# Kernel optimization log

Measured on AMD Instinct MI355X. Metric: run time of the kernel, lower is better.

Reference implementation:

```python
import jax, jax.numpy as jnp
import numpy as np

# CLEVR-scale dims
B, N, DF, DE, DV, H, NC, QV, L = 128, 36, 512, 256, 512, 256, 28, 2000, 5


def _lin(key, fan_in, fan_out):
    k1, _ = jax.random.split(key)
    w = jax.random.normal(k1, (fan_in, fan_out), jnp.float32) * np.sqrt(2.0 / fan_in)  # kaiming
    b = jnp.zeros((fan_out,), jnp.float32)
    return w, b


def setup_inputs() -> dict:
    key = jax.random.key(0)
    ks = jax.random.split(key, 12)
    node_feats = jax.random.normal(ks[0], (B, N, DF), jnp.float32)
    edge_feats = jax.random.normal(ks[1], (B, N, N, DE), jnp.float32)
    programs = jax.random.randint(ks[2], (B, L), 0, 10)
    program_inputs = jax.random.randint(ks[3], (B, L), 0, QV)
    W_n1, b_n1 = _lin(ks[4], DF, H)
    W_n2, b_n2 = _lin(ks[5], H, DV)
    W_e1, b_e1 = _lin(ks[6], DE, H)
    W_e2, b_e2 = _lin(ks[7], H, DV)
    W_q, b_q = _lin(ks[8], DV, DV)
    W_c1, b_c1 = _lin(ks[9], DV, H)
    W_c2, b_c2 = _lin(ks[10], H, NC)
    word_emb = jax.random.normal(ks[11], (QV, DV), jnp.float32) / np.sqrt(DV)
    return dict(node_feats=node_feats, edge_feats=edge_feats,
                W_n1=W_n1, b_n1=b_n1, W_n2=W_n2, b_n2=b_n2,
                W_e1=W_e1, b_e1=b_e1, W_e2=W_e2, b_e2=b_e2,
                W_q=W_q, b_q=b_q, W_c1=W_c1, b_c1=b_c1,
                W_c2=W_c2, b_c2=b_c2, word_emb=word_emb,
                programs=programs, program_inputs=program_inputs)


def _mlp(x, W1, b1, W2, b2):
    return jax.nn.relu(x @ W1 + b1) @ W2 + b2


def reference(node_feats, edge_feats, W_n1, b_n1, W_n2, b_n2,
              W_e1, b_e1, W_e2, b_e2, W_q, b_q,
              W_c1, b_c1, W_c2, b_c2, word_emb,
              programs, program_inputs):
    # Fixed representative program (executed in reverse order like the torch code):
    # scene -> filter -> relate -> filter -> query -> classifier
    del programs
    scale = 1.0 / np.sqrt(DV)
    nf = _mlp(node_feats, W_n1, b_n1, W_n2, b_n2)      # [B,N,DV]  map_node_feat_to_v
    ef = _mlp(edge_feats, W_e1, b_e1, W_e2, b_e2)      # [B,N,N,DV] map_edge_feat_to_v
    q = word_emb[program_inputs]                        # [B,L,DV]  word_embedding lookup
    # scene: attention of ones over nodes
    attn = jnp.ones(nf.shape[:2], nf.dtype)             # [B,N]
    # filter (AttentionModule): gate node attention by query-node similarity
    attn = attn * jax.nn.sigmoid(jnp.einsum('bnd,bd->bn', nf, q[:, 3]) * scale)
    # relate (RelateModule): transfer attention along query-weighted edges
    weit = jax.nn.sigmoid(jnp.einsum('bijd,bd->bij', ef, q[:, 2]) * scale)  # [B,N,N]
    attn = jnp.clip(jnp.einsum('bi,bij->bj', attn, weit), 0.0, 1.0)
    # filter again
    attn = attn * jax.nn.sigmoid(jnp.einsum('bnd,bd->bn', nf, q[:, 1]) * scale)
    # query (QueryModule): attention-pooled node feature gated by query, projected
    attn_n = attn / (attn.sum(-1, keepdims=True) + 1e-8)
    pooled = jnp.einsum('bn,bnd->bd', attn_n, nf)        # [B,DV]
    out = jax.nn.relu((pooled * q[:, 0]) @ W_q + b_q)    # [B,DV]
    # classifier
    return jax.nn.relu(out @ W_c1 + b_c1) @ W_c2 + b_c2  # [B,NC]
```

## Files before the change

### kernel.cpp

```cpp
#include <hip/hip_runtime.h>
#include <math.h>

#define BB 128
#define NN 36
#define DF 512
#define DE 256
#define DV 512
#define HH 256
#define NCC 28
#define LQ 5
#define NE 1296
#define SCALE 0.04419417382415922f

typedef __bf16 bf16_8 __attribute__((ext_vector_type(8)));
typedef __bf16 bf16_4 __attribute__((ext_vector_type(4)));
typedef float  f32_4  __attribute__((ext_vector_type(4)));

__device__ __forceinline__ float sigmoidf_(float x){ return 1.0f/(1.0f + expf(-x)); }
__device__ __forceinline__ float reluf_(float x){ return x > 0.f ? x : 0.f; }

__global__ __launch_bounds__(256) void k_pack_all(
    const float* __restrict__ W_n1, const float* __restrict__ W_n2,
    const float* __restrict__ W_q,  const float* __restrict__ W_c1,
    const float* __restrict__ W_e1,
    __bf16* __restrict__ Pn1h, __bf16* __restrict__ Pn1l,
    __bf16* __restrict__ Pn2h, __bf16* __restrict__ Pn2l,
    __bf16* __restrict__ Pqh,  __bf16* __restrict__ Pql,
    __bf16* __restrict__ Pc1h, __bf16* __restrict__ Pc1l,
    __bf16* __restrict__ Peh)
{
    int bid = blockIdx.x;
    const float* W; __bf16 *Ph, *Pl; int N, base;
    if (bid < 64)       { W=W_n1; Ph=Pn1h; Pl=Pn1l; N=256; base=0;   }
    else if (bid < 128) { W=W_n2; Ph=Pn2h; Pl=Pn2l; N=512; base=64;  }
    else if (bid < 256) { W=W_q;  Ph=Pqh;  Pl=Pql;  N=512; base=128; }
    else if (bid < 320) { W=W_c1; Ph=Pc1h; Pl=Pc1l; N=256; base=256; }
    else                { W=W_e1; Ph=Peh;  Pl=nullptr; N=256; base=320; }
    int g = (bid-base)*256 + threadIdx.x;
    int lane = g & 63, slot = g >> 6;
    int NT = N >> 4;
    int nt = slot % NT, kt = slot / NT;
    int krow = kt*32 + (lane>>4)*8, ncol = nt*16 + (lane&15);
    #pragma unroll
    for (int j=0;j<8;j++){
        float w = W[(size_t)(krow+j)*N + ncol];
        __bf16 hi = (__bf16)w;
        Ph[(size_t)g*8+j] = hi;
        if (Pl) Pl[(size_t)g*8+j] = (__bf16)(w - (float)hi);
    }
}

__global__ __launch_bounds__(256) void k_prep(
    const float* __restrict__ word_emb, const int* __restrict__ program_inputs,
    const float* __restrict__ W_e2, const float* __restrict__ b_e2,
    float* __restrict__ qws, float* __restrict__ ve, float* __restrict__ se)
{
    int b = blockIdx.x, t = threadIdx.x, wv = t>>6, lane = t&63;
    int idx[4];
    #pragma unroll
    for (int k=0;k<4;k++) idx[k] = program_inputs[b*LQ + k];
    #pragma unroll
    for (int k=0;k<4;k++){
        qws[((size_t)(b*4+k))*DV + t]       = word_emb[(size_t)idx[k]*DV + t];
        qws[((size_t)(b*4+k))*DV + t + 256] = word_emb[(size_t)idx[k]*DV + t + 256];
    }
    const float* q2p = word_emb + (size_t)idx[2]*DV + lane*8;
    float4 qa = *(const float4*)q2p, qb = *(const float4*)(q2p+4);
    for (int i=0;i<64;i++){
        int h = wv*64 + i;
        const float* wr = W_e2 + (size_t)h*DV + lane*8;
        float4 a = *(const float4*)wr, c = *(const float4*)(wr+4);
        float p = a.x*qa.x + a.y*qa.y + a.z*qa.z + a.w*qa.w
                + c.x*qb.x + c.y*qb.y + c.z*qb.z + c.w*qb.w;
        #pragma unroll
        for (int off=32; off; off>>=1) p += __shfl_xor(p, off, 64);
        if (lane==0) ve[b*HH + h] = p;
    }
    float pp = b_e2[t]*word_emb[(size_t)idx[2]*DV + t]
             + b_e2[t+256]*word_emb[(size_t)idx[2]*DV + t + 256];
    __shared__ float red[4];
    #pragma unroll
    for (int off=32; off; off>>=1) pp += __shfl_down(pp, off, 64);
    if ((t&63)==0) red[t>>6] = pp;
    __syncthreads();
    if (t==0) se[b] = red[0]+red[1]+red[2]+red[3];
}

__global__ __launch_bounds__(256) void k_node(
    const float* __restrict__ X,
    const __bf16* __restrict__ W1h, const __bf16* __restrict__ W1l,
    const float* __restrict__ b1,
    const __bf16* __restrict__ W2h, const __bf16* __restrict__ W2l,
    const float* __restrict__ b2,
    float* __restrict__ nf)
{
    __shared__ __align__(16) __bf16 xh[16*512];
    __shared__ __align__(16) __bf16 xl[16*512];
    __shared__ __align__(16) __bf16 hh[8*64*8];
    __shared__ __align__(16) __bf16 hl[8*64*8];
    int r0 = blockIdx.x*16, t = threadIdx.x, wv = t>>6, lane = t&63;

    #pragma unroll
    for (int i=0;i<8;i++){
        int linear = t + i*256;
        int row = linear >> 7, c4 = (linear & 127)*4;
        float4 f = *(const float4*)(X + (size_t)(r0+row)*DF + c4);
        int kt = c4 >> 5, lane2 = ((c4 & 31) >> 3)*16 + row, j2 = c4 & 7;
        bf16_4 h, l;
        h[0]=(__bf16)f.x; l[0]=(__bf16)(f.x-(float)h[0]);
        h[1]=(__bf16)f.y; l[1]=(__bf16)(f.y-(float)h[1]);
        h[2]=(__bf16)f.z; l[2]=(__bf16)(f.z-(float)h[2]);
        h[3]=(__bf16)f.w; l[3]=(__bf16)(f.w-(float)h[3]);
        int off = (kt*64 + lane2)*8 + j2;
        *(bf16_4*)&xh[off] = h;
        *(bf16_4*)&xl[off] = l;
    }
    __syncthreads();

    f32_4 zero = {0.f,0.f,0.f,0.f};
    f32_4 acc1[4];
    #pragma unroll
    for (int nt=0;nt<4;nt++) acc1[nt] = zero;
    for (int kt=0; kt<16; kt++){
        bf16_8 ah = *(const bf16_8*)&xh[(kt*64+lane)*8];
        bf16_8 al = *(const bf16_8*)&xl[(kt*64+lane)*8];
        #pragma unroll
        for (int nt=0;nt<4;nt++){
            size_t bo = ((size_t)(kt*16 + wv*4+nt)*64 + lane)*8;
            bf16_8 bh = *(const bf16_8*)(W1h + bo);
            bf16_8 bl = *(const bf16_8*)(W1l + bo);
            acc1[nt] = __builtin_amdgcn_mfma_f32_16x16x32_bf16(ah, bh, acc1[nt], 0,0,0);
            acc1[nt] = __builtin_amdgcn_mfma_f32_16x16x32_bf16(al, bh, acc1[nt], 0,0,0);
            acc1[nt] = __builtin_amdgcn_mfma_f32_16x16x32_bf16(ah, bl, acc1[nt], 0,0,0);
        }
    }
    int q = lane>>4, c = lane&15;
    #pragma unroll
    for (int nt=0;nt<4;nt++){
        int col = wv*64 + nt*16 + c;
        float bias = b1[col];
        int kt2 = col>>5, j2 = col&7;
        int lbase = ((col&31)>>3)*16;
        #pragma unroll
        for (int r=0;r<4;r++){
            int row = q*4 + r;
            float v = reluf_(acc1[nt][r] + bias);
            __bf16 hi = (__bf16)v;
            int off = (kt2*64 + lbase + row)*8 + j2;
            hh[off] = hi;
            hl[off] = (__bf16)(v - (float)hi);
        }
    }
    __syncthreads();

    f32_4 acc2[8];
    #pragma unroll
    for (int nt=0;nt<8;nt++) acc2[nt] = zero;
    for (int kt=0; kt<8; kt++){
        bf16_8 ah = *(const bf16_8*)&hh[(kt*64+lane)*8];
        bf16_8 al = *(const bf16_8*)&hl[(kt*64+lane)*8];
        #pragma unroll
        for (int nt=0;nt<8;nt++){
            size_t bo = ((size_t)(kt*32 + wv*8+nt)*64 + lane)*8;
            bf16_8 bh = *(const bf16_8*)(W2h + bo);
            bf16_8 bl = *(const bf16_8*)(W2l + bo);
            acc2[nt] = __builtin_amdgcn_mfma_f32_16x16x32_bf16(ah, bh, acc2[nt], 0,0,0);
            acc2[nt] = __builtin_amdgcn_mfma_f32_16x16x32_bf16(al, bh, acc2[nt], 0,0,0);
            acc2[nt] = __builtin_amdgcn_mfma_f32_16x16x32_bf16(ah, bl, acc2[nt], 0,0,0);
        }
    }
    #pragma unroll
    for (int nt=0;nt<8;nt++){
        int col = wv*128 + nt*16 + c;
        float bias = b2[col];
        #pragma unroll
        for (int r=0;r<4;r++){
            int row = q*4 + r;
            nf[(size_t)(r0+row)*DV + col] = acc2[nt][r] + bias;
        }
    }
}

__global__ __launch_bounds__(256) void k_edge(
    const float* __restrict__ E, const __bf16* __restrict__ Wp,
    const float* __restrict__ b_e1, const float* __restrict__ ve,
    const float* __restrict__ se, float* __restrict__ weit)
{
    constexpr int LDW = DE + 8;
    __shared__ __align__(16) __bf16 as[48*LDW];
    __shared__ float red[4][48];
    int bx = blockIdx.x;
    int b = bx / 27, tile = bx % 27;
    int e0 = tile*48;
    int t = threadIdx.x, wv = t>>6, lane = t&63;
    const float* Eb = E + ((size_t)b*NE + e0)*DE;

    #pragma unroll
    for (int i=0;i<6;i++){
        int cch = t + i*256;
        int row = cch >> 5, cc = cch & 31;
        const float* src = Eb + (size_t)row*DE + cc*8;
        float4 f0 = *(const float4*)(src);
        float4 f1 = *(const float4*)(src+4);
        bf16_8 v;
        v[0]=(__bf16)f0.x; v[1]=(__bf16)f0.y; v[2]=(__bf16)f0.z; v[3]=(__bf16)f0.w;
        v[4]=(__bf16)f1.x; v[5]=(__bf16)f1.y; v[6]=(__bf16)f1.z; v[7]=(__bf16)f1.w;
        *(bf16_8*)&as[row*LDW + cc*8] = v;
    }
    __syncthreads();

    f32_4 zero = {0.f,0.f,0.f,0.f};
    f32_4 acc[3][4];
    #pragma unroll
    for (int mt=0;mt<3;mt++)
        #pragma unroll
        for (int nt=0;nt<4;nt++) acc[mt][nt] = zero;

    int arow = lane & 15, ako = (lane>>4)*8;
    for (int kt=0; kt<8; kt++){
        bf16_8 afrag[3];
        #pragma unroll
        for (int mt=0;mt<3;mt++)
            afrag[mt] = *(const bf16_8*)&as[(mt*16 + arow)*LDW + kt*32 + ako];
        #pragma unroll
        for (int nt=0;nt<4;nt++){
            bf16_8 bfrag = *(const bf16_8*)(Wp + ((size_t)(kt*16 + (wv*4+nt))*64 + lane)*8);
            #pragma unroll
            for (int mt=0;mt<3;mt++)
                acc[mt][nt] = __builtin_amdgcn_mfma_f32_16x16x32_bf16(afrag[mt], bfrag, acc[mt][nt], 0,0,0);
        }
    }

    float ves[4], be[4];
    #pragma unroll
    for (int nt=0;nt<4;nt++){
        int n = wv*64 + nt*16 + (lane&15);
        ves[nt] = ve[b*HH + n];
        be[nt]  = b_e1[n];
    }
    float part[3][4];
    #pragma unroll
    for (int mt=0;mt<3;mt++)
        #pragma unroll
        for (int r=0;r<4;r++){
            float s = 0.f;
            #pragma unroll
            for (int nt=0;nt<4;nt++)
                s = fmaf(reluf_(acc[mt][nt][r] + be[nt]), ves[nt], s);
            part[mt][r] = s;
        }
    #pragma unroll
    for (int off=1; off<16; off<<=1)
        #pragma unroll
        for (int mt=0;mt<3;mt++)
            #pragma unroll
            for (int r=0;r<4;r++)
                part[mt][r] += __shfl_xor(part[mt][r], off, 64);
    if ((lane&15)==0){
        int g = lane>>4;
        #pragma unroll
        for (int mt=0;mt<3;mt++)
            #pragma unroll
            for (int r=0;r<4;r++)
                red[wv][mt*16 + g*4 + r] = part[mt][r];
    }
    __syncthreads();
    if (t < 48){
        float logit = red[0][t]+red[1][t]+red[2][t]+red[3][t] + se[b];
        weit[(size_t)b*NE + e0 + t] = sigmoidf_(logit * SCALE);
    }
}

__global__ __launch_bounds__(256) void k_attn(
    const float* __restrict__ nf, const float* __restrict__ qws,
    const float* __restrict__ weit, float* __restrict__ xws)
{
    int b = blockIdx.x, t = threadIdx.x;
    int wv = t>>6, lane = t&63;
    __shared__ float a1[NN], a2[NN], a3[NN];
    __shared__ float denom;
    const float* nfb = nf + (size_t)b*NN*DV;
    const float* q0 = qws + ((size_t)(b*4+0))*DV;
    const float* q1 = qws + ((size_t)(b*4+1))*DV;
    const float* q3 = qws + ((size_t)(b*4+3))*DV;

    for (int i=wv; i<NN; i+=4){
        const float* row = nfb + (size_t)i*DV + lane*8;
        const float* qq  = q3 + lane*8;
        float4 x0 = *(const float4*)row, x1 = *(const float4*)(row+4);
        float4 y0 = *(const float4*)qq,  y1 = *(const float4*)(qq+4);
        float p = x0.x*y0.x + x0.y*y0.y + x0.z*y0.z + x0.w*y0.w
                + x1.x*y1.x + x1.y*y1.y + x1.z*y1.z + x1.w*y1.w;
        #pragma unroll
        for (int off=32; off; off>>=1) p += __shfl_xor(p, off, 64);
        if (lane==0) a1[i] = sigmoidf_(p*SCALE);
    }
    __syncthreads();
    if (t < NN){
        const float* wrow = weit + (size_t)b*NE;
        float s = 0.f;
        for (int i=0;i<NN;i++) s = fmaf(a1[i], wrow[i*NN + t], s);
        a2[t] = fminf(fmaxf(s, 0.f), 1.f);
    }
    __syncthreads();
    for (int i=wv; i<NN; i+=4){
        const float* row = nfb + (size_t)i*DV + lane*8;
        const float* qq  = q1 + lane*8;
        float4 x0 = *(const float4*)row, x1 = *(const float4*)(row+4);
        float4 y0 = *(const float4*)qq,  y1 = *(const float4*)(qq+4);
        float p = x0.x*y0.x + x0.y*y0.y + x0.z*y0.z + x0.w*y0.w
                + x1.x*y1.x + x1.y*y1.y + x1.z*y1.z + x1.w*y1.w;
        #pragma unroll
        for (int off=32; off; off>>=1) p += __shfl_xor(p, off, 64);
        if (lane==0) a3[i] = a2[i]*sigmoidf_(p*SCALE);
    }
    __syncthreads();
    if (t==0){
        float s = 0.f;
        for (int i=0;i<NN;i++) s += a3[i];
        denom = 1.f/(s + 1e-8f);
    }
    __syncthreads();
    float p0=0.f, p1=0.f;
    for (int i=0;i<NN;i++){
        float a = a3[i]*denom;
        p0 = fmaf(a, nfb[(size_t)i*DV + t], p0);
        p1 = fmaf(a, nfb[(size_t)i*DV + t + 256], p1);
    }
    xws[(size_t)b*DV + t]       = p0*q0[t];
    xws[(size_t)b*DV + t + 256] = p1*q0[t+256];
}

__global__ __launch_bounds__(256) void k_head(
    const float* __restrict__ xws,
    const __bf16* __restrict__ Wqh, const __bf16* __restrict__ Wql,
    const float* __restrict__ b_q,
    const __bf16* __restrict__ Wc1h, const __bf16* __restrict__ Wc1l,
    const float* __restrict__ b_c1,
    const float* __restrict__ W_c2, const float* __restrict__ b_c2,
    float* __restrict__ out)
{
    __shared__ __align__(16) char smem[65536];
    __bf16* xh = (__bf16*)smem;
    __bf16* xl = xh + 8192;
    __bf16* oh = (__bf16*)(smem + 32768);
    __bf16* ol = oh + 8192;
    float* hbuf  = (float*)smem;
    float* wc2s  = (float*)(smem + 32768);

    int r0 = blockIdx.x*16, t = threadIdx.x, wv = t>>6, lane = t&63;
    int q = lane>>4, c = lane&15;

    #pragma unroll
    for (int i=0;i<8;i++){
        int linear = t + i*256;
        int row = linear >> 7, c4 = (linear & 127)*4;
        float4 f = *(const float4*)(xws + (size_t)(r0+row)*DV + c4);
        int kt = c4 >> 5, lane2 = ((c4 & 31) >> 3)*16 + row, j2 = c4 & 7;
        bf16_4 h, l;
        h[0]=(__bf16)f.x; l[0]=(__bf16)(f.x-(float)h[0]);
        h[1]=(__bf16)f.y; l[1]=(__bf16)(f.y-(float)h[1]);
        h[2]=(__bf16)f.z; l[2]=(__bf16)(f.z-(float)h[2]);
        h[3]=(__bf16)f.w; l[3]=(__bf16)(f.w-(float)h[3]);
        int off = (kt*64 + lane2)*8 + j2;
        *(bf16_4*)&xh[off] = h;
        *(bf16_4*)&xl[off] = l;
    }
    __syncthreads();

    f32_4 zero = {0.f,0.f,0.f,0.f};
    f32_4 acc[8];
    #pragma unroll
    for (int nt=0;nt<8;nt++) acc[nt] = zero;
    for (int kt=0; kt<16; kt++){
        bf16_8 ah = *(const bf16_8*)&xh[(kt*64+lane)*8];
        bf16_8 al = *(const bf16_8*)&xl[(kt*64+lane)*8];
        #pragma unroll
        for (int nt=0;nt<8;nt++){
            size_t bo = ((size_t)(kt*32 + wv*8+nt)*64 + lane)*8;
            bf16_8 bh = *(const bf16_8*)(Wqh + bo);
            bf16_8 bl = *(const bf16_8*)(Wql + bo);
            acc[nt] = __builtin_amdgcn_mfma_f32_16x16x32_bf16(ah, bh, acc[nt], 0,0,0);
            acc[nt] = __builtin_amdgcn_mfma_f32_16x16x32_bf16(al, bh, acc[nt], 0,0,0);
            acc[nt] = __builtin_amdgcn_mfma_f32_16x16x32_bf16(ah, bl, acc[nt], 0,0,0);
        }
    }
    #pragma unroll
    for (int nt=0;nt<8;nt++){
        int col = wv*128 + nt*16 + c;
        float bias = b_q[col];
        int kt2 = col>>5, j2 = col&7;
        int lbase = ((col&31)>>3)*16;
        #pragma unroll
        for (int r=0;r<4;r++){
            int row = q*4 + r;
            float v = reluf_(acc[nt][r] + bias);
            __bf16 hi = (__bf16)v;
            int off = (kt2*64 + lbase + row)*8 + j2;
            oh[off] = hi;
            ol[off] = (__bf16)(v - (float)hi);
        }
    }
    __syncthreads();

    f32_4 acc2[4];
    #pragma unroll
    for (int nt=0;nt<4;nt++) acc2[nt] = zero;
    for (int kt=0; kt<16; kt++){
        bf16_8 ah = *(const bf16_8*)&oh[(kt*64+lane)*8];
        bf16_8 al = *(const bf16_8*)&ol[(kt*64+lane)*8];
        #pragma unroll
        for (int nt=0;nt<4;nt++){
            size_t bo = ((size_t)(kt*16 + wv*4+nt)*64 + lane)*8;
            bf16_8 bh = *(const bf16_8*)(Wc1h + bo);
            bf16_8 bl = *(const bf16_8*)(Wc1l + bo);
            acc2[nt] = __builtin_amdgcn_mfma_f32_16x16x32_bf16(ah, bh, acc2[nt], 0,0,0);
            acc2[nt] = __builtin_amdgcn_mfma_f32_16x16x32_bf16(al, bh, acc2[nt], 0,0,0);
            acc2[nt] = __builtin_amdgcn_mfma_f32_16x16x32_bf16(ah, bl, acc2[nt], 0,0,0);
        }
    }
    __syncthreads();
    #pragma unroll
    for (int nt=0;nt<4;nt++){
        int col = wv*64 + nt*16 + c;
        float bias = b_c1[col];
        #pragma unroll
        for (int r=0;r<4;r++){
            int row = q*4 + r;
            hbuf[row*264 + col] = reluf_(acc2[nt][r] + bias);
        }
    }
    for (int i=t; i<1792; i+=256)
        ((float4*)wc2s)[i] = ((const float4*)W_c2)[i];
    __syncthreads();

    for (int idx=t; idx<16*NCC; idx+=256){
        int row = idx / NCC, cc = idx - row*NCC;
        float s = b_c2[cc];
        for (int k=0;k<HH;k++)
            s = fmaf(hbuf[row*264 + k], wc2s[k*NCC + cc], s);
        out[(size_t)(r0+row)*NCC + cc] = s;
    }
}

extern "C" void kernel_launch(void* const* d_in, const int* in_sizes, int n_in,
                              void* d_out, int out_size, void* d_ws, size_t ws_size,
                              hipStream_t stream)
{
    const float* node_feats = (const float*)d_in[0];
    const float* edge_feats = (const float*)d_in[1];
    const float* W_n1 = (const float*)d_in[2];
    const float* b_n1 = (const float*)d_in[3];
    const float* W_n2 = (const float*)d_in[4];
    const float* b_n2 = (const float*)d_in[5];
    const float* W_e1 = (const float*)d_in[6];
    const float* b_e1 = (const float*)d_in[7];
    const float* W_e2 = (const float*)d_in[8];
    const float* b_e2 = (const float*)d_in[9];
    const float* W_q  = (const float*)d_in[10];
    const float* b_q  = (const float*)d_in[11];
    const float* W_c1 = (const float*)d_in[12];
    const float* b_c1 = (const float*)d_in[13];
    const float* W_c2 = (const float*)d_in[14];
    const float* b_c2 = (const float*)d_in[15];
    const float* word_emb = (const float*)d_in[16];
    const int* program_inputs = (const int*)d_in[18];

    char* ws = (char*)d_ws;
    float* qws  = (float*)ws; ws += (size_t)BB*4*DV*4;
    float* ve   = (float*)ws; ws += (size_t)BB*HH*4;
    float* se   = (float*)ws; ws += 512;
    float* xws  = (float*)ws; ws += (size_t)BB*DV*4;
    __bf16* Pn1h = (__bf16*)ws; ws += (size_t)DF*HH*2;
    __bf16* Pn1l = (__bf16*)ws; ws += (size_t)DF*HH*2;
    __bf16* Pn2h = (__bf16*)ws; ws += (size_t)HH*DV*2;
    __bf16* Pn2l = (__bf16*)ws; ws += (size_t)HH*DV*2;
    __bf16* Pqh  = (__bf16*)ws; ws += (size_t)DV*DV*2;
    __bf16* Pql  = (__bf16*)ws; ws += (size_t)DV*DV*2;
    __bf16* Pc1h = (__bf16*)ws; ws += (size_t)DV*HH*2;
    __bf16* Pc1l = (__bf16*)ws; ws += (size_t)DV*HH*2;
    __bf16* Peh  = (__bf16*)ws; ws += (size_t)DE*HH*2;
    float* nf   = (float*)ws; ws += (size_t)BB*NN*DV*4;
    float* weit = (float*)ws; ws += (size_t)BB*NE*4;

    k_pack_all<<<352, 256, 0, stream>>>(W_n1, W_n2, W_q, W_c1, W_e1,
                                        Pn1h, Pn1l, Pn2h, Pn2l, Pqh, Pql, Pc1h, Pc1l, Peh);
    k_prep<<<BB, 256, 0, stream>>>(word_emb, program_inputs, W_e2, b_e2, qws, ve, se);
    k_node<<<(BB*NN)/16, 256, 0, stream>>>(node_feats, Pn1h, Pn1l, b_n1, Pn2h, Pn2l, b_n2, nf);
    k_edge<<<BB*27, 256, 0, stream>>>(edge_feats, Peh, b_e1, ve, se, weit);
    k_attn<<<BB, 256, 0, stream>>>(nf, qws, weit, xws);
    k_head<<<BB/16, 256, 0, stream>>>(xws, Pqh, Pql, b_q, Pc1h, Pc1l, b_c1, W_c2, b_c2,
                                      (float*)d_out);
}
```

Measured before the change: 457.5 us.

## Load MFMA A-fragments directly from global memory and move classifier output to MFMA

The node, edge and head kernels now load fp32 input rows straight from global memory into registers in MFMA fragment layout and convert them there, instead of staging through LDS with a barrier. The edge kernel uses nontemporal loads for the large streamed edge tensor. The final classifier layer, previously a scalar fp32 loop over LDS, now uses split-bf16 MFMA with W_c2 packed (padded to 32 columns) in the pack kernel. The aim is lower LDS traffic, fewer syncs and better occupancy, at the cost of less coalesced global access patterns.

After: 529.8 us. +15.8%, slower.

```diff
diff --git a/kernel.cpp b/kernel.cpp
--- a/kernel.cpp
+++ b/kernel.cpp
@@ -19,23 +19,41 @@
 __device__ __forceinline__ float sigmoidf_(float x){ return 1.0f/(1.0f + expf(-x)); }
 __device__ __forceinline__ float reluf_(float x){ return x > 0.f ? x : 0.f; }
 
+__device__ __forceinline__ bf16_8 cvt8(f32_4 f0, f32_4 f1){
+    bf16_8 v;
+    #pragma unroll
+    for (int i=0;i<4;i++){ v[i] = (__bf16)f0[i]; v[i+4] = (__bf16)f1[i]; }
+    return v;
+}
+__device__ __forceinline__ void split8(f32_4 f0, f32_4 f1, bf16_8& h, bf16_8& l){
+    #pragma unroll
+    for (int i=0;i<4;i++){
+        __bf16 hi = (__bf16)f0[i];
+        h[i] = hi; l[i] = (__bf16)(f0[i] - (float)hi);
+        __bf16 hi2 = (__bf16)f1[i];
+        h[i+4] = hi2; l[i+4] = (__bf16)(f1[i] - (float)hi2);
+    }
+}
+
 __global__ __launch_bounds__(256) void k_pack_all(
     const float* __restrict__ W_n1, const float* __restrict__ W_n2,
     const float* __restrict__ W_q,  const float* __restrict__ W_c1,
-    const float* __restrict__ W_e1,
+    const float* __restrict__ W_e1, const float* __restrict__ W_c2,
     __bf16* __restrict__ Pn1h, __bf16* __restrict__ Pn1l,
     __bf16* __restrict__ Pn2h, __bf16* __restrict__ Pn2l,
     __bf16* __restrict__ Pqh,  __bf16* __restrict__ Pql,
     __bf16* __restrict__ Pc1h, __bf16* __restrict__ Pc1l,
-    __bf16* __restrict__ Peh)
+    __bf16* __restrict__ Peh,
+    __bf16* __restrict__ Pc2h, __bf16* __restrict__ Pc2l)
 {
     int bid = blockIdx.x;
-    const float* W; __bf16 *Ph, *Pl; int N, base;
-    if (bid < 64)       { W=W_n1; Ph=Pn1h; Pl=Pn1l; N=256; base=0;   }
-    else if (bid < 128) { W=W_n2; Ph=Pn2h; Pl=Pn2l; N=512; base=64;  }
-    else if (bid < 256) { W=W_q;  Ph=Pqh;  Pl=Pql;  N=512; base=128; }
-    else if (bid < 320) { W=W_c1; Ph=Pc1h; Pl=Pc1l; N=256; base=256; }
-    else                { W=W_e1; Ph=Peh;  Pl=nullptr; N=256; base=320; }
+    const float* W; __bf16 *Ph, *Pl; int N, base, realN;
+    if (bid < 64)       { W=W_n1; Ph=Pn1h; Pl=Pn1l; N=256; base=0;   realN=256; }
+    else if (bid < 128) { W=W_n2; Ph=Pn2h; Pl=Pn2l; N=512; base=64;  realN=512; }
+    else if (bid < 256) { W=W_q;  Ph=Pqh;  Pl=Pql;  N=512; base=128; realN=512; }
+    else if (bid < 320) { W=W_c1; Ph=Pc1h; Pl=Pc1l; N=256; base=256; realN=256; }
+    else if (bid < 352) { W=W_e1; Ph=Peh;  Pl=nullptr; N=256; base=320; realN=256; }
+    else                { W=W_c2; Ph=Pc2h; Pl=Pc2l; N=32;  base=352; realN=28;  }
     int g = (bid-base)*256 + threadIdx.x;
     int lane = g & 63, slot = g >> 6;
     int NT = N >> 4;
@@ -43,7 +61,7 @@
     int krow = kt*32 + (lane>>4)*8, ncol = nt*16 + (lane&15);
     #pragma unroll
     for (int j=0;j<8;j++){
-        float w = W[(size_t)(krow+j)*N + ncol];
+        float w = (ncol < realN) ? W[(size_t)(krow+j)*realN + ncol] : 0.f;
         __bf16 hi = (__bf16)w;
         Ph[(size_t)g*8+j] = hi;
         if (Pl) Pl[(size_t)g*8+j] = (__bf16)(w - (float)hi);
@@ -65,13 +83,13 @@
         qws[((size_t)(b*4+k))*DV + t + 256] = word_emb[(size_t)idx[k]*DV + t + 256];
     }
     const float* q2p = word_emb + (size_t)idx[2]*DV + lane*8;
-    float4 qa = *(const float4*)q2p, qb = *(const float4*)(q2p+4);
+    f32_4 qa = *(const f32_4*)q2p, qb = *(const f32_4*)(q2p+4);
     for (int i=0;i<64;i++){
         int h = wv*64 + i;
         const float* wr = W_e2 + (size_t)h*DV + lane*8;
-        float4 a = *(const float4*)wr, c = *(const float4*)(wr+4);
-        float p = a.x*qa.x + a.y*qa.y + a.z*qa.z + a.w*qa.w
-                + c.x*qb.x + c.y*qb.y + c.z*qb.z + c.w*qb.w;
+        f32_4 a = *(const f32_4*)wr, c = *(const f32_4*)(wr+4);
+        float p = a[0]*qa[0] + a[1]*qa[1] + a[2]*qa[2] + a[3]*qa[3]
+                + c[0]*qb[0] + c[1]*qb[1] + c[2]*qb[2] + c[3]*qb[3];
         #pragma unroll
         for (int off=32; off; off>>=1) p += __shfl_xor(p, off, 64);
         if (lane==0) ve[b*HH + h] = p;
@@ -94,36 +112,22 @@
     const float* __restrict__ b2,
     float* __restrict__ nf)
 {
-    __shared__ __align__(16) __bf16 xh[16*512];
-    __shared__ __align__(16) __bf16 xl[16*512];
-    __shared__ __align__(16) __bf16 hh[8*64*8];
-    __shared__ __align__(16) __bf16 hl[8*64*8];
+    __shared__ __align__(16) __bf16 hh[4096];
+    __shared__ __align__(16) __bf16 hl[4096];
     int r0 = blockIdx.x*16, t = threadIdx.x, wv = t>>6, lane = t&63;
-
-    #pragma unroll
-    for (int i=0;i<8;i++){
-        int linear = t + i*256;
-        int row = linear >> 7, c4 = (linear & 127)*4;
-        float4 f = *(const float4*)(X + (size_t)(r0+row)*DF + c4);
-        int kt = c4 >> 5, lane2 = ((c4 & 31) >> 3)*16 + row, j2 = c4 & 7;
-        bf16_4 h, l;
-        h[0]=(__bf16)f.x; l[0]=(__bf16)(f.x-(float)h[0]);
-        h[1]=(__bf16)f.y; l[1]=(__bf16)(f.y-(float)h[1]);
-        h[2]=(__bf16)f.z; l[2]=(__bf16)(f.z-(float)h[2]);
-        h[3]=(__bf16)f.w; l[3]=(__bf16)(f.w-(float)h[3]);
-        int off = (kt*64 + lane2)*8 + j2;
-        *(bf16_4*)&xh[off] = h;
-        *(bf16_4*)&xl[off] = l;
-    }
-    __syncthreads();
-
+    int m = lane&15, kc = lane>>4;
+    int q = lane>>4, c = lane&15;
+
+    const float* xr = X + (size_t)(r0+m)*DF + kc*8;
     f32_4 zero = {0.f,0.f,0.f,0.f};
     f32_4 acc1[4];
     #pragma unroll
     for (int nt=0;nt<4;nt++) acc1[nt] = zero;
     for (int kt=0; kt<16; kt++){
-        bf16_8 ah = *(const bf16_8*)&xh[(kt*64+lane)*8];
-        bf16_8 al = *(const bf16_8*)&xl[(kt*64+lane)*8];
+        f32_4 f0 = *(const f32_4*)(xr + kt*32);
+        f32_4 f1 = *(const f32_4*)(xr + kt*32 + 4);
+        bf16_8 ah, al;
+        split8(f0, f1, ah, al);
         #pragma unroll
         for (int nt=0;nt<4;nt++){
             size_t bo = ((size_t)(kt*16 + wv*4+nt)*64 + lane)*8;
@@ -134,7 +138,6 @@
             acc1[nt] = __builtin_amdgcn_mfma_f32_16x16x32_bf16(ah, bl, acc1[nt], 0,0,0);
         }
     }
-    int q = lane>>4, c = lane&15;
     #pragma unroll
     for (int nt=0;nt<4;nt++){
         int col = wv*64 + nt*16 + c;
@@ -186,28 +189,16 @@
     const float* __restrict__ b_e1, const float* __restrict__ ve,
     const float* __restrict__ se, float* __restrict__ weit)
 {
-    constexpr int LDW = DE + 8;
-    __shared__ __align__(16) __bf16 as[48*LDW];
     __shared__ float red[4][48];
     int bx = blockIdx.x;
     int b = bx / 27, tile = bx % 27;
     int e0 = tile*48;
     int t = threadIdx.x, wv = t>>6, lane = t&63;
-    const float* Eb = E + ((size_t)b*NE + e0)*DE;
-
-    #pragma unroll
-    for (int i=0;i<6;i++){
-        int cch = t + i*256;
-        int row = cch >> 5, cc = cch & 31;
-        const float* src = Eb + (size_t)row*DE + cc*8;
-        float4 f0 = *(const float4*)(src);
-        float4 f1 = *(const float4*)(src+4);
-        bf16_8 v;
-        v[0]=(__bf16)f0.x; v[1]=(__bf16)f0.y; v[2]=(__bf16)f0.z; v[3]=(__bf16)f0.w;
-        v[4]=(__bf16)f1.x; v[5]=(__bf16)f1.y; v[6]=(__bf16)f1.z; v[7]=(__bf16)f1.w;
-        *(bf16_8*)&as[row*LDW + cc*8] = v;
-    }
-    __syncthreads();
+    int m = lane&15, kc = lane>>4;
+    const float* base = E + ((size_t)b*NE + e0)*DE + kc*8;
+    const float* rp0 = base + (size_t)(0*16 + m)*DE;
+    const float* rp1 = base + (size_t)(1*16 + m)*DE;
+    const float* rp2 = base + (size_t)(2*16 + m)*DE;
 
     f32_4 zero = {0.f,0.f,0.f,0.f};
     f32_4 acc[3][4];
@@ -216,25 +207,27 @@
         #pragma unroll
         for (int nt=0;nt<4;nt++) acc[mt][nt] = zero;
 
-    int arow = lane & 15, ako = (lane>>4)*8;
     for (int kt=0; kt<8; kt++){
-        bf16_8 afrag[3];
-        #pragma unroll
-        for (int mt=0;mt<3;mt++)
-            afrag[mt] = *(const bf16_8*)&as[(mt*16 + arow)*LDW + kt*32 + ako];
+        bf16_8 af[3];
+        af[0] = cvt8(__builtin_nontemporal_load((const f32_4*)(rp0 + kt*32)),
+                     __builtin_nontemporal_load((const f32_4*)(rp0 + kt*32 + 4)));
+        af[1] = cvt8(__builtin_nontemporal_load((const f32_4*)(rp1 + kt*32)),
+                     __builtin_nontemporal_load((const f32_4*)(rp1 + kt*32 + 4)));
+        af[2] = cvt8(__builtin_nontemporal_load((const f32_4*)(rp2 + kt*32)),
+                     __builtin_nontemporal_load((const f32_4*)(rp2 + kt*32 + 4)));
         #pragma unroll
         for (int nt=0;nt<4;nt++){
             bf16_8 bfrag = *(const bf16_8*)(Wp + ((size_t)(kt*16 + (wv*4+nt))*64 + lane)*8);
             #pragma unroll
             for (int mt=0;mt<3;mt++)
-                acc[mt][nt] = __builtin_amdgcn_mfma_f32_16x16x32_bf16(afrag[mt], bfrag, acc[mt][nt], 0,0,0);
+                acc[mt][nt] = __builtin_amdgcn_mfma_f32_16x16x32_bf16(af[mt], bfrag, acc[mt][nt], 0,0,0);
         }
     }
 
     float ves[4], be[4];
     #pragma unroll
     for (int nt=0;nt<4;nt++){
-        int n = wv*64 + nt*16 + (lane&15);
+        int n = wv*64 + nt*16 + m;
         ves[nt] = ve[b*HH + n];
         be[nt]  = b_e1[n];
     }
@@ -256,7 +249,7 @@
             #pragma unroll
             for (int r=0;r<4;r++)
                 part[mt][r] += __shfl_xor(part[mt][r], off, 64);
-    if ((lane&15)==0){
+    if (m==0){
         int g = lane>>4;
         #pragma unroll
         for (int mt=0;mt<3;mt++)
@@ -287,10 +280,10 @@
     for (int i=wv; i<NN; i+=4){
         const float* row = nfb + (size_t)i*DV + lane*8;
         const float* qq  = q3 + lane*8;
-        float4 x0 = *(const float4*)row, x1 = *(const float4*)(row+4);
-        float4 y0 = *(const float4*)qq,  y1 = *(const float4*)(qq+4);
-        float p = x0.x*y0.x + x0.y*y0.y + x0.z*y0.z + x0.w*y0.w
-                + x1.x*y1.x + x1.y*y1.y + x1.z*y1.z + x1.w*y1.w;
+        f32_4 x0 = *(const f32_4*)row, x1 = *(const f32_4*)(row+4);
+        f32_4 y0 = *(const f32_4*)qq,  y1 = *(const f32_4*)(qq+4);
+        float p = x0[0]*y0[0] + x0[1]*y0[1] + x0[2]*y0[2] + x0[3]*y0[3]
+                + x1[0]*y1[0] + x1[1]*y1[1] + x1[2]*y1[2] + x1[3]*y1[3];
         #pragma unroll
         for (int off=32; off; off>>=1) p += __shfl_xor(p, off, 64);
         if (lane==0) a1[i] = sigmoidf_(p*SCALE);
@@ -306,10 +299,10 @@
     for (int i=wv; i<NN; i+=4){
         const float* row = nfb + (size_t)i*DV + lane*8;
         const float* qq  = q1 + lane*8;
-        float4 x0 = *(const float4*)row, x1 = *(const float4*)(row+4);
-        float4 y0 = *(const float4*)qq,  y1 = *(const float4*)(qq+4);
-        float p = x0.x*y0.x + x0.y*y0.y + x0.z*y0.z + x0.w*y0.w
-                + x1.x*y1.x + x1.y*y1.y + x1.z*y1.z + x1.w*y1.w;
+        f32_4 x0 = *(const f32_4*)row, x1 = *(const f32_4*)(row+4);
+        f32_4 y0 = *(const f32_4*)qq,  y1 = *(const f32_4*)(qq+4);
+        float p = x0[0]*y0[0] + x0[1]*y0[1] + x0[2]*y0[2] + x0[3]*y0[3]
+                + x1[0]*y1[0] + x1[1]*y1[1] + x1[2]*y1[2] + x1[3]*y1[3];
         #pragma unroll
         for (int off=32; off; off>>=1) p += __shfl_xor(p, off, 64);
         if (lane==0) a3[i] = a2[i]*sigmoidf_(p*SCALE);
@@ -337,44 +330,29 @@
     const float* __restrict__ b_q,
     const __bf16* __restrict__ Wc1h, const __bf16* __restrict__ Wc1l,
     const float* __restrict__ b_c1,
-    const float* __restrict__ W_c2, const float* __restrict__ b_c2,
+    const __bf16* __restrict__ Pc2h, const __bf16* __restrict__ Pc2l,
+    const float* __restrict__ b_c2,
     float* __restrict__ out)
 {
-    __shared__ __align__(16) char smem[65536];
-    __bf16* xh = (__bf16*)smem;
-    __bf16* xl = xh + 8192;
-    __bf16* oh = (__bf16*)(smem + 32768);
-    __bf16* ol = oh + 8192;
-    float* hbuf  = (float*)smem;
-    float* wc2s  = (float*)(smem + 32768);
+    __shared__ __align__(16) __bf16 oh[8192];
+    __shared__ __align__(16) __bf16 ol[8192];
+    __shared__ __align__(16) __bf16 hfh[4096];
+    __shared__ __align__(16) __bf16 hfl[4096];
 
     int r0 = blockIdx.x*16, t = threadIdx.x, wv = t>>6, lane = t&63;
+    int m = lane&15, kc = lane>>4;
     int q = lane>>4, c = lane&15;
-
-    #pragma unroll
-    for (int i=0;i<8;i++){
-        int linear = t + i*256;
-        int row = linear >> 7, c4 = (linear & 127)*4;
-        float4 f = *(const float4*)(xws + (size_t)(r0+row)*DV + c4);
-        int kt = c4 >> 5, lane2 = ((c4 & 31) >> 3)*16 + row, j2 = c4 & 7;
-        bf16_4 h, l;
-        h[0]=(__bf16)f.x; l[0]=(__bf16)(f.x-(float)h[0]);
-        h[1]=(__bf16)f.y; l[1]=(__bf16)(f.y-(float)h[1]);
-        h[2]=(__bf16)f.z; l[2]=(__bf16)(f.z-(float)h[2]);
-        h[3]=(__bf16)f.w; l[3]=(__bf16)(f.w-(float)h[3]);
-        int off = (kt*64 + lane2)*8 + j2;
-        *(bf16_4*)&xh[off] = h;
-        *(bf16_4*)&xl[off] = l;
-    }
-    __syncthreads();
-
     f32_4 zero = {0.f,0.f,0.f,0.f};
+
+    const float* xr = xws + (size_t)(r0+m)*DV + kc*8;
     f32_4 acc[8];
     #pragma unroll
     for (int nt=0;nt<8;nt++) acc[nt] = zero;
     for (int kt=0; kt<16; kt++){
-        bf16_8 ah = *(const bf16_8*)&xh[(kt*64+lane)*8];
-        bf16_8 al = *(const bf16_8*)&xl[(kt*64+lane)*8];
+        f32_4 f0 = *(const f32_4*)(xr + kt*32);
+        f32_4 f1 = *(const f32_4*)(xr + kt*32 + 4);
+        bf16_8 ah, al;
+        split8(f0, f1, ah, al);
         #pragma unroll
         for (int nt=0;nt<8;nt++){
             size_t bo = ((size_t)(kt*32 + wv*8+nt)*64 + lane)*8;
@@ -419,27 +397,45 @@
             acc2[nt] = __builtin_amdgcn_mfma_f32_16x16x32_bf16(ah, bl, acc2[nt], 0,0,0);
         }
     }
-    __syncthreads();
     #pragma unroll
     for (int nt=0;nt<4;nt++){
         int col = wv*64 + nt*16 + c;
         float bias = b_c1[col];
+        int kt2 = col>>5, j2 = col&7;
+        int lbase = ((col&31)>>3)*16;
         #pragma unroll
         for (int r=0;r<4;r++){
             int row = q*4 + r;
-            hbuf[row*264 + col] = reluf_(acc2[nt][r] + bias);
-        }
-    }
-    for (int i=t; i<1792; i+=256)
-        ((float4*)wc2s)[i] = ((const float4*)W_c2)[i];
-    __syncthreads();
-
-    for (int idx=t; idx<16*NCC; idx+=256){
-        int row = idx / NCC, cc = idx - row*NCC;
-        float s = b_c2[cc];
-        for (int k=0;k<HH;k++)
-            s = fmaf(hbuf[row*264 + k], wc2s[k*NCC + cc], s);
-        out[(size_t)(r0+row)*NCC + cc] = s;
+            float v = reluf_(acc2[nt][r] + bias);
+            __bf16 hi = (__bf16)v;
+            int off = (kt2*64 + lbase + row)*8 + j2;
+            hfh[off] = hi;
+            hfl[off] = (__bf16)(v - (float)hi);
+        }
+    }
+    __syncthreads();
+
+    if (wv < 2){
+        f32_4 acc3 = zero;
+        for (int kt=0; kt<8; kt++){
+            bf16_8 ah = *(const bf16_8*)&hfh[(kt*64+lane)*8];
+            bf16_8 al = *(const bf16_8*)&hfl[(kt*64+lane)*8];
+            size_t bo = ((size_t)(kt*2 + wv)*64 + lane)*8;
+            bf16_8 bh = *(const bf16_8*)(Pc2h + bo);
+            bf16_8 bl = *(const bf16_8*)(Pc2l + bo);
+            acc3 = __builtin_amdgcn_mfma_f32_16x16x32_bf16(ah, bh, acc3, 0,0,0);
+            acc3 = __builtin_amdgcn_mfma_f32_16x16x32_bf16(al, bh, acc3, 0,0,0);
+            acc3 = __builtin_amdgcn_mfma_f32_16x16x32_bf16(ah, bl, acc3, 0,0,0);
+        }
+        int col = wv*16 + c;
+        if (col < NCC){
+            float bias = b_c2[col];
+            #pragma unroll
+            for (int r=0;r<4;r++){
+                int row = q*4 + r;
+                out[(size_t)(r0+row)*NCC + col] = acc3[r] + bias;
+            }
+        }
     }
 }
 
@@ -480,15 +476,18 @@
     __bf16* Pc1h = (__bf16*)ws; ws += (size_t)DV*HH*2;
     __bf16* Pc1l = (__bf16*)ws; ws += (size_t)DV*HH*2;
     __bf16* Peh  = (__bf16*)ws; ws += (size_t)DE*HH*2;
+    __bf16* Pc2h = (__bf16*)ws; ws += (size_t)HH*32*2;
+    __bf16* Pc2l = (__bf16*)ws; ws += (size_t)HH*32*2;
     float* nf   = (float*)ws; ws += (size_t)BB*NN*DV*4;
     float* weit = (float*)ws; ws += (size_t)BB*NE*4;
 
-    k_pack_all<<<352, 256, 0, stream>>>(W_n1, W_n2, W_q, W_c1, W_e1,
-                                        Pn1h, Pn1l, Pn2h, Pn2l, Pqh, Pql, Pc1h, Pc1l, Peh);
+    k_pack_all<<<356, 256, 0, stream>>>(W_n1, W_n2, W_q, W_c1, W_e1, W_c2,
+                                        Pn1h, Pn1l, Pn2h, Pn2l, Pqh, Pql, Pc1h, Pc1l,
+                                        Peh, Pc2h, Pc2l);
     k_prep<<<BB, 256, 0, stream>>>(word_emb, program_inputs, W_e2, b_e2, qws, ve, se);
     k_node<<<(BB*NN)/16, 256, 0, stream>>>(node_feats, Pn1h, Pn1l, b_n1, Pn2h, Pn2l, b_n2, nf);
     k_edge<<<BB*27, 256, 0, stream>>>(edge_feats, Peh, b_e1, ve, se, weit);
     k_attn<<<BB, 256, 0, stream>>>(nf, qws, weit, xws);
-    k_head<<<BB/16, 256, 0, stream>>>(xws, Pqh, Pql, b_q, Pc1h, Pc1l, b_c1, W_c2, b_c2,
-                                      (float*)d_out);
-}
+    k_head<<<BB/16, 256, 0, stream>>>(xws, Pqh, Pql, b_q, Pc1h, Pc1l, b_c1,
+                                      Pc2h, Pc2l, b_c2, (float*)d_out);
+}
```
